# Kernel optimization log

Hardware: AMD Instinct MI355X
Metric: run time of the kernel (lower is better)

Reference implementation:

```python
import jax, jax.numpy as jnp
import numpy as np

N = 100000
IN_C = 256
OUT_C = 256
E = 500000


def gcn_conv(x, W, b, edges):
    """PyG GCNConv: add self-loops, symmetric D^-1/2 (A+I) D^-1/2 normalization,
    then scatter-add of transformed source features into targets, plus bias."""
    n = x.shape[0]
    loop = jnp.arange(n, dtype=edges.dtype)
    row = jnp.concatenate([edges[0], loop])  # source
    col = jnp.concatenate([edges[1], loop])  # target
    deg = jax.ops.segment_sum(jnp.ones_like(col, dtype=x.dtype), col, num_segments=n)
    dis = jax.lax.rsqrt(deg)  # deg >= 1 after self-loops
    norm = dis[row] * dis[col]  # [E+n]
    h = x @ W  # [n, out]
    msg = h[row] * norm[:, None]  # gather + scale
    return jax.ops.segment_sum(msg, col, num_segments=n) + b


def setup_inputs() -> dict:
    key = jax.random.key(0)
    ks = jax.random.split(key, 24)
    x = jax.random.normal(ks[0], (N, IN_C), dtype=jnp.float32)
    edges00 = jax.random.randint(ks[1], (2, E), 0, N, dtype=jnp.int32)
    edges01 = jax.random.randint(ks[2], (2, E), 0, N, dtype=jnp.int32)
    edges10 = jax.random.randint(ks[3], (2, E), 0, N, dtype=jnp.int32)
    edges11 = jax.random.randint(ks[4], (2, E), 0, N, dtype=jnp.int32)
    t0 = (jax.random.uniform(ks[5], (N,)) > 0.5).astype(jnp.float32)
    t1 = 1.0 - t0
    scale = 1.0 / np.sqrt(IN_C)
    W1 = jax.random.normal(ks[6], (IN_C, OUT_C), dtype=jnp.float32) * scale
    W2 = jax.random.normal(ks[7], (IN_C, OUT_C), dtype=jnp.float32) * scale
    W3 = jax.random.normal(ks[8], (IN_C, OUT_C), dtype=jnp.float32) * scale
    W4 = jax.random.normal(ks[9], (IN_C, OUT_C), dtype=jnp.float32) * scale
    b1 = jnp.zeros((OUT_C,), jnp.float32)
    b2 = jnp.zeros((OUT_C,), jnp.float32)
    b3 = jnp.zeros((OUT_C,), jnp.float32)
    b4 = jnp.zeros((OUT_C,), jnp.float32)
    p0 = jax.random.normal(ks[10], (OUT_C,), dtype=jnp.float32)
    p1 = jax.random.normal(ks[11], (OUT_C,), dtype=jnp.float32)
    p2 = jax.random.normal(ks[12], (OUT_C,), dtype=jnp.float32)
    p3 = jax.random.normal(ks[13], (OUT_C,), dtype=jnp.float32)
    p4 = jax.random.normal(ks[14], (OUT_C,), dtype=jnp.float32)
    p5 = jax.random.normal(ks[15], (OUT_C,), dtype=jnp.float32)
    return dict(x=x, edges00=edges00, edges01=edges01, edges10=edges10, edges11=edges11,
                type0_idx=t0, type1_idx=t1,
                W1=W1, b1=b1, W2=W2, b2=b2, W3=W3, b3=b3, W4=W4, b4=b4,
                p0=p0, p1=p1, p2=p2, p3=p3, p4=p4, p5=p5)


def reference(x, edges00, edges01, edges10, edges11, type0_idx, type1_idx,
              W1, b1, W2, b2, W3, b3, W4, b4, p0, p1, p2, p3, p4, p5):
    # x0/x1: first feature column masked by node type, broadcast over out channels
    x0c = type0_idx * x[:, 0]  # [N]
    x1c = type1_idx * x[:, 0]
    x00 = gcn_conv(x, W1, b1, edges00)
    x01 = gcn_conv(x, W2, b2, edges01)
    x10 = gcn_conv(x, W3, b3, edges10)
    x11 = gcn_conv(x, W4, b4, edges11)
    out = (x0c[:, None] * p0 + x1c[:, None] * p1
           + x00 * p2 + x01 * p3 + x10 * p4 + x11 * p5)
    return out
```

## Files before the change

kernel.cpp:

```cpp
#include <hip/hip_runtime.h>


#define PCAP 24

typedef __bf16 v8bf __attribute__((ext_vector_type(8)));
typedef float v4f __attribute__((ext_vector_type(4)));

__device__ __forceinline__ unsigned short f2bf(float f) {
  unsigned u = __float_as_uint(f);
  u += 0x7fffu + ((u >> 16) & 1u);
  return (unsigned short)(u >> 16);
}
__device__ __forceinline__ float bf2f(unsigned short s) {
  return __uint_as_float(((unsigned)s) << 16);
}
__device__ __forceinline__ void async_ld16(const void* g, void* l) {
  __builtin_amdgcn_global_load_lds((__attribute__((address_space(1))) void*)g,
                                   (__attribute__((address_space(3))) void*)l,
                                   16, 0, 0);
}

__global__ void lc_hist(const int* __restrict__ e0, const int* __restrict__ e1,
                        const int* __restrict__ e2, const int* __restrict__ e3,
                        int* __restrict__ deg, int N, int E) {
  int e = blockIdx.x * 256 + threadIdx.x;
  if (e >= E) return;
  int k = blockIdx.y;
  const int* ed = (k == 0) ? e0 : (k == 1) ? e1 : (k == 2) ? e2 : e3;
  int col = ed[E + e];
  atomicAdd(&deg[k * N + col], 1);
}

__global__ void lc_fill(const int* __restrict__ e0, const int* __restrict__ e1,
                        const int* __restrict__ e2, const int* __restrict__ e3,
                        const int* __restrict__ deg, int* __restrict__ cursor,
                        unsigned* __restrict__ payload, int N, int E) {
  int e = blockIdx.x * 256 + threadIdx.x;
  if (e >= E) return;
  int k = blockIdx.y;
  const int* ed = (k == 0) ? e0 : (k == 1) ? e1 : (k == 2) ? e2 : e3;
  int src = ed[e], col = ed[E + e];
  int idx = k * N + col;
  int pos = atomicAdd(&cursor[idx], 1);
  if (pos < PCAP) {
    float ds = rsqrtf((float)(deg[(size_t)k * N + src] + 1));
    unsigned q = (unsigned)(ds * 32767.0f + 0.5f);
    payload[(size_t)idx * PCAP + pos] = (q << 17) | (unsigned)src;
  }
}

__global__ void lc_prep(const float* __restrict__ W1, const float* __restrict__ W2,
                        const float* __restrict__ W3, const float* __restrict__ W4,
                        const float* __restrict__ b1, const float* __restrict__ b2,
                        const float* __restrict__ b3, const float* __restrict__ b4,
                        const float* __restrict__ p2, const float* __restrict__ p3,
                        const float* __restrict__ p4, const float* __restrict__ p5,
                        unsigned short* __restrict__ Wt, float* __restrict__ biasc) {
  __shared__ float tile[256][33];
  int k = blockIdx.y, co0 = blockIdx.x * 32;
  int t = threadIdx.x;
  const float* W = (k == 0) ? W1 : (k == 1) ? W2 : (k == 2) ? W3 : W4;
  const float* p = (k == 0) ? p2 : (k == 1) ? p3 : (k == 2) ? p4 : p5;

  if (blockIdx.x == 0 && k == 0) {
    int c = t;
    biasc[c] = b1[c] * p2[c] + b2[c] * p3[c] + b3[c] * p4[c] + b4[c] * p5[c];
  }

  int coL = t & 31, kkB = t >> 5;
#pragma unroll 4
  for (int pass = 0; pass < 32; ++pass) {
    int kk = pass * 8 + kkB;
    tile[kk][coL] = W[kk * 256 + co0 + coL];
  }
  __syncthreads();

  int co = t >> 3, seg0 = t & 7;
  float pv = p[co0 + co];
#pragma unroll
  for (int i = 0; i < 4; ++i) {
    int s = seg0 + 8 * i;
    ushort4 lo, hi;
    int kk = s * 8;
    lo.x = f2bf(tile[kk + 0][co] * pv); lo.y = f2bf(tile[kk + 1][co] * pv);
    lo.z = f2bf(tile[kk + 2][co] * pv); lo.w = f2bf(tile[kk + 3][co] * pv);
    hi.x = f2bf(tile[kk + 4][co] * pv); hi.y = f2bf(tile[kk + 5][co] * pv);
    hi.z = f2bf(tile[kk + 6][co] * pv); hi.w = f2bf(tile[kk + 7][co] * pv);
    unsigned short* dst = Wt + (size_t)(co0 + co) * 1024 + k * 256 + kk;
    *(ushort4*)dst = lo;
    *(ushort4*)(dst + 4) = hi;
  }
}

__global__ void lc_cvt(const float4* __restrict__ x4, ushort4* __restrict__ xb4,
                       const float* __restrict__ t0, const float* __restrict__ t1,
                       float* __restrict__ m0, float* __restrict__ m1, int n4) {
  int i = blockIdx.x * 256 + threadIdx.x;
  if (i >= n4) return;
  float4 v = x4[i];
  ushort4 r;
  r.x = f2bf(v.x); r.y = f2bf(v.y); r.z = f2bf(v.z); r.w = f2bf(v.w);
  xb4[i] = r;
  if ((i & 63) == 0) {
    int n = i >> 6;
    float xc = v.x;
    m0[n] = t0[n] * xc;
    m1[n] = t1[n] * xc;
  }
}

#define GATP(BASE, POS, LIM, CNT, DNS, A0, A1, A2, A3)                  \
  do {                                                                  \
    int jj = ((POS) < (CNT)) ? (POS) : (LIM);                           \
    unsigned pv = payload[(BASE) + jj];                                 \
    unsigned ss = pv & 0x1FFFFu;                                        \
    ushort4 gg = *(const ushort4*)&xb[(size_t)ss * 256 + c];            \
    float nn = ((POS) < (CNT)) ? (float)(pv >> 17) * (DNS) : 0.f;       \
    A0 += bf2f(gg.x) * nn;                                              \
    A1 += bf2f(gg.y) * nn;                                              \
    A2 += bf2f(gg.z) * nn;                                              \
    A3 += bf2f(gg.w) * nn;                                              \
  } while (0)

__global__ __launch_bounds__(256) void lc_aggx(
    const unsigned short* __restrict__ xb, unsigned short* __restrict__ Agg,
    int aggw, int kcount, int kbase, const int* __restrict__ deg,
    const unsigned* __restrict__ payload, int N) {
  int t = threadIdx.x;
  int w = t >> 6, lane = t & 63;
  int n0, k, koff;
  if (kcount == 4) { n0 = blockIdx.x * 2; k = w; koff = k * 256; }
  else { n0 = blockIdx.x * 8 + w * 2; k = kbase; koff = 0; }
  if (n0 >= N) return;
  int c = lane * 4;
  int n1 = n0 + 1;
  int n1c = (n1 < N) ? n1 : N - 1;
  int idx0 = k * N + n0;
  int idx1 = k * N + n1c;

  int dg0 = deg[idx0], dg1 = deg[idx1];
  float dn0 = rsqrtf((float)(dg0 + 1)), dn1 = rsqrtf((float)(dg1 + 1));
  float dns0 = dn0 * (1.0f / 32767.0f), dns1 = dn1 * (1.0f / 32767.0f);
  float s0 = dn0 * dn0, s1 = dn1 * dn1;
  ushort4 h0 = *(const ushort4*)&xb[(size_t)n0 * 256 + c];
  ushort4 h1 = *(const ushort4*)&xb[(size_t)n1c * 256 + c];
  float a0 = bf2f(h0.x) * s0, a1 = bf2f(h0.y) * s0;
  float a2 = bf2f(h0.z) * s0, a3 = bf2f(h0.w) * s0;
  float u0 = bf2f(h1.x) * s1, u1 = bf2f(h1.y) * s1;
  float u2 = bf2f(h1.z) * s1, u3 = bf2f(h1.w) * s1;

  size_t st0 = (size_t)idx0 * PCAP, st1 = (size_t)idx1 * PCAP;
  int cnt0 = (dg0 > PCAP) ? PCAP : dg0;
  int cnt1 = (dg1 > PCAP) ? PCAP : dg1;
  int lim0 = (cnt0 > 0) ? cnt0 - 1 : 0;
  int lim1 = (cnt1 > 0) ? cnt1 - 1 : 0;
  int cmax = (cnt0 > cnt1) ? cnt0 : cnt1;
  for (int i = 0; i < cmax; i += 4) {
    GATP(st0, i + 0, lim0, cnt0, dns0, a0, a1, a2, a3);
    GATP(st0, i + 1, lim0, cnt0, dns0, a0, a1, a2, a3);
    GATP(st0, i + 2, lim0, cnt0, dns0, a0, a1, a2, a3);
    GATP(st0, i + 3, lim0, cnt0, dns0, a0, a1, a2, a3);
    GATP(st1, i + 0, lim1, cnt1, dns1, u0, u1, u2, u3);
    GATP(st1, i + 1, lim1, cnt1, dns1, u0, u1, u2, u3);
    GATP(st1, i + 2, lim1, cnt1, dns1, u0, u1, u2, u3);
    GATP(st1, i + 3, lim1, cnt1, dns1, u0, u1, u2, u3);
  }

  ushort4 r0, r1;
  r0.x = f2bf(a0); r0.y = f2bf(a1); r0.z = f2bf(a2); r0.w = f2bf(a3);
  r1.x = f2bf(u0); r1.y = f2bf(u1); r1.z = f2bf(u2); r1.w = f2bf(u3);
  *(ushort4*)&Agg[(size_t)n0 * aggw + koff + c] = r0;
  if (n1 < N) *(ushort4*)&Agg[(size_t)n1 * aggw + koff + c] = r1;
}

__global__ __launch_bounds__(512) void lc_gemm(
    const unsigned short* __restrict__ A, int strideA,
    const unsigned short* __restrict__ B, int strideB, int K,
    float* __restrict__ out, int Mrows, int addprev, int doepi,
    const float* __restrict__ m0, const float* __restrict__ m1,
    const float* __restrict__ p0, const float* __restrict__ p1,
    const float* __restrict__ biasc) {
  __shared__ alignas(16) unsigned short As[2][128 * 32];
  __shared__ alignas(16) unsigned short Bs[2][256 * 32];
  int t = threadIdx.x;
  int w = t >> 6, lane = t & 63;
  int wm = w & 1, wn = w >> 1;
  int quad = lane >> 4, l16 = lane & 15;
  int row0 = blockIdx.x * 128;

  v4f acc[4][4];
#pragma unroll
  for (int mt = 0; mt < 4; mt++)
#pragma unroll
    for (int nt = 0; nt < 4; nt++) {
      v4f z = {0.f, 0.f, 0.f, 0.f};
      acc[mt][nt] = z;
    }

  const int ra = t >> 2;
  const int e0 = (t & 3) * 8;
  const int sws = (ra & 3) << 3;
  const unsigned swf = (unsigned)((l16 & 3) << 3);

  int growA = row0 + ra;
  if (growA >= Mrows) growA = Mrows - 1;
  const unsigned short* Ap = A + (size_t)growA * strideA + (e0 ^ sws);
  const unsigned short* Bp0 = B + (size_t)ra * strideB + (e0 ^ sws);
  const unsigned short* Bp1 = B + (size_t)(128 + ra) * strideB + (e0 ^ sws);
  const int lA = ra * 32 + e0;
  const int lB0 = ra * 32 + e0, lB1 = (128 + ra) * 32 + e0;

  async_ld16(Ap, &As[0][lA]);
  async_ld16(Bp0, &Bs[0][lB0]);
  async_ld16(Bp1, &Bs[0][lB1]);
  asm volatile("s_waitcnt vmcnt(0)" ::: "memory");
  __builtin_amdgcn_s_barrier();

  int cur = 0;
  for (int kk = 0; kk < K; kk += 32) {
    if (kk + 32 < K) {
      async_ld16(Ap + kk + 32, &As[cur ^ 1][lA]);
      async_ld16(Bp0 + kk + 32, &Bs[cur ^ 1][lB0]);
      async_ld16(Bp1 + kk + 32, &Bs[cur ^ 1][lB1]);
    }

    v8bf af[4], bfr[4];
    unsigned eq = ((unsigned)(quad * 8)) ^ swf;
#pragma unroll
    for (int mt = 0; mt < 4; mt++) {
      int r = wm * 64 + mt * 16 + l16;
      af[mt] = *(const v8bf*)&As[cur][(unsigned)r * 32 + eq];
    }
#pragma unroll
    for (int nt = 0; nt < 4; nt++) {
      int n = wn * 64 + nt * 16 + l16;
      bfr[nt] = *(const v8bf*)&Bs[cur][(unsigned)n * 32 + eq];
    }
#pragma unroll
    for (int mt = 0; mt < 4; mt++)
#pragma unroll
      for (int nt = 0; nt < 4; nt++)
        acc[mt][nt] =
            __builtin_amdgcn_mfma_f32_16x16x32_bf16(af[mt], bfr[nt], acc[mt][nt], 0, 0, 0);

    asm volatile("s_waitcnt vmcnt(0)" ::: "memory");
    __builtin_amdgcn_s_barrier();
    cur ^= 1;
  }

  float pc0[4], pc1[4], bc[4];
#pragma unroll
  for (int nt = 0; nt < 4; nt++) {
    int gcol = wn * 64 + nt * 16 + l16;
    pc0[nt] = doepi ? p0[gcol] : 0.f;
    pc1[nt] = doepi ? p1[gcol] : 0.f;
    bc[nt] = doepi ? biasc[gcol] : 0.f;
  }
#pragma unroll
  for (int mt = 0; mt < 4; mt++)
#pragma unroll
    for (int r = 0; r < 4; r++) {
      int grow = row0 + wm * 64 + mt * 16 + quad * 4 + r;
      if (grow >= Mrows) continue;
      float m0v = 0.f, m1v = 0.f;
      if (doepi) { m0v = m0[grow]; m1v = m1[grow]; }
#pragma unroll
      for (int nt = 0; nt < 4; nt++) {
        int gcol = wn * 64 + nt * 16 + l16;
        size_t o = (size_t)grow * 256 + gcol;
        float v = acc[mt][nt][r];
        if (addprev) v += out[o];
        if (doepi) v += m0v * pc0[nt] + m1v * pc1[nt] + bc[nt];
        out[o] = v;
      }
    }
}

extern "C" void kernel_launch(void* const* d_in, const int* in_sizes, int n_in,
                              void* d_out, int out_size, void* d_ws, size_t ws_size,
                              hipStream_t stream) {
  const float* x = (const float*)d_in[0];
  const int* e00 = (const int*)d_in[1];
  const int* e01 = (const int*)d_in[2];
  const int* e10 = (const int*)d_in[3];
  const int* e11 = (const int*)d_in[4];
  const float* t0 = (const float*)d_in[5];
  const float* t1 = (const float*)d_in[6];
  const float* W1 = (const float*)d_in[7];
  const float* b1 = (const float*)d_in[8];
  const float* W2 = (const float*)d_in[9];
  const float* b2 = (const float*)d_in[10];
  const float* W3 = (const float*)d_in[11];
  const float* b3 = (const float*)d_in[12];
  const float* W4 = (const float*)d_in[13];
  const float* b4 = (const float*)d_in[14];
  const float* p0 = (const float*)d_in[15];
  const float* p1 = (const float*)d_in[16];
  const float* p2 = (const float*)d_in[17];
  const float* p3 = (const float*)d_in[18];
  const float* p4 = (const float*)d_in[19];
  const float* p5 = (const float*)d_in[20];
  float* out = (float*)d_out;

  int N = in_sizes[0] / 256;
  int E = in_sizes[1] / 2;
  int M4 = 4 * N;

  char* wp = (char*)d_ws;
  auto carve = [&](size_t bytes) {
    void* r = (void*)wp;
    wp += (bytes + 255) & ~(size_t)255;
    return r;
  };
  unsigned short* xb = (unsigned short*)carve((size_t)N * 256 * 2);
  unsigned short* Wt = (unsigned short*)carve((size_t)256 * 1024 * 2);
  int* deg = (int*)carve((size_t)M4 * 4);
  int* cursor = (int*)carve((size_t)M4 * 4);
  float* biasc = (float*)carve(256 * 4);
  float* m0 = (float*)carve((size_t)N * 4);
  float* m1 = (float*)carve((size_t)N * 4);
  unsigned* payload = (unsigned*)carve((size_t)M4 * PCAP * 4);
  size_t used = (size_t)(wp - (char*)d_ws);
  size_t remain = (ws_size > used) ? ws_size - used : 0;
  bool fat = remain >= (size_t)N * 1024 * 2;
  unsigned short* Agg = (unsigned short*)wp;

  int gE = (E + 255) / 256;

  hipMemsetAsync(deg, 0, (size_t)2 * M4 * 4, stream);
  lc_hist<<<dim3(gE, 4), 256, 0, stream>>>(e00, e01, e10, e11, deg, N, E);
  lc_fill<<<dim3(gE, 4), 256, 0, stream>>>(e00, e01, e10, e11, deg, cursor,
                                           payload, N, E);
  lc_prep<<<dim3(8, 4), 256, 0, stream>>>(W1, W2, W3, W4, b1, b2, b3, b4,
                                          p2, p3, p4, p5, Wt, biasc);
  lc_cvt<<<(N * 64 + 255) / 256, 256, 0, stream>>>((const float4*)x, (ushort4*)xb,
                                                   t0, t1, m0, m1, N * 64);

  int gemm_mb = (N + 127) / 128;
  if (fat) {
    lc_aggx<<<(N + 1) / 2, 256, 0, stream>>>(xb, Agg, 1024, 4, 0, deg, payload, N);
    lc_gemm<<<gemm_mb, 512, 0, stream>>>(Agg, 1024, Wt, 1024, 1024, out, N,
                                         0, 1, m0, m1, p0, p1, biasc);
  } else {
    for (int k = 0; k < 4; k++) {
      lc_aggx<<<(N + 7) / 8, 256, 0, stream>>>(xb, Agg, 256, 1, k, deg, payload, N);
      lc_gemm<<<gemm_mb, 512, 0, stream>>>(Agg, 256, Wt + k * 256, 1024, 256,
                                           out, N, (k > 0) ? 1 : 0,
                                           (k == 3) ? 1 : 0, m0, m1, p0, p1,
                                           biasc);
    }
  }
}
```

Measured before the change: 690.6 us.

## Merge preprocessing kernels into one launch and triple-buffer GEMM loads

The histogram, bf16 conversion and weight-prep kernels are folded into a single launch that dispatches work by block index, removing two kernel launches. The weight transpose now uses one block per output column with strided, uncoalesced reads instead of an LDS tile. The GEMM moves from a double-buffered to a triple-buffered LDS pipeline with partial vmcnt waits, so loads run two tiles ahead. This uses more shared memory per block, which may reduce occupancy.

```diff
diff --git a/kernel.cpp b/kernel.cpp
--- a/kernel.cpp
+++ b/kernel.cpp
@@ -20,15 +20,57 @@
                                    16, 0, 0);
 }
 
-__global__ void lc_hist(const int* __restrict__ e0, const int* __restrict__ e1,
-                        const int* __restrict__ e2, const int* __restrict__ e3,
-                        int* __restrict__ deg, int N, int E) {
-  int e = blockIdx.x * 256 + threadIdx.x;
-  if (e >= E) return;
-  int k = blockIdx.y;
-  const int* ed = (k == 0) ? e0 : (k == 1) ? e1 : (k == 2) ? e2 : e3;
-  int col = ed[E + e];
-  atomicAdd(&deg[k * N + col], 1);
+__global__ void lc_pre(const int* __restrict__ e0, const int* __restrict__ e1,
+                       const int* __restrict__ e2, const int* __restrict__ e3,
+                       int* __restrict__ deg, int N, int E, int gE,
+                       const float4* __restrict__ x4, ushort4* __restrict__ xb4,
+                       const float* __restrict__ t0, const float* __restrict__ t1,
+                       float* __restrict__ m0, float* __restrict__ m1,
+                       const float* __restrict__ W1, const float* __restrict__ W2,
+                       const float* __restrict__ W3, const float* __restrict__ W4,
+                       const float* __restrict__ b1, const float* __restrict__ b2,
+                       const float* __restrict__ b3, const float* __restrict__ b4,
+                       const float* __restrict__ p2, const float* __restrict__ p3,
+                       const float* __restrict__ p4, const float* __restrict__ p5,
+                       unsigned short* __restrict__ Wt, float* __restrict__ biasc) {
+  int b = blockIdx.x;
+  int tid = threadIdx.x;
+  int HB = 4 * gE;
+  int CB = (N * 64 + 255) / 256;
+
+  if (b < HB) {
+    int k = b / gE;
+    int e = (b - k * gE) * 256 + tid;
+    if (e >= E) return;
+    const int* ed = (k == 0) ? e0 : (k == 1) ? e1 : (k == 2) ? e2 : e3;
+    atomicAdd(&deg[k * N + ed[E + e]], 1);
+    return;
+  }
+  b -= HB;
+  if (b < CB) {
+    int i = b * 256 + tid;
+    if (i >= N * 64) return;
+    float4 v = x4[i];
+    ushort4 r;
+    r.x = f2bf(v.x); r.y = f2bf(v.y); r.z = f2bf(v.z); r.w = f2bf(v.w);
+    xb4[i] = r;
+    if ((i & 63) == 0) {
+      int n = i >> 6;
+      float xc = v.x;
+      m0[n] = t0[n] * xc;
+      m1[n] = t1[n] * xc;
+    }
+    return;
+  }
+  b -= CB;
+  int k = b >> 8, co = b & 255;
+  const float* W = (k == 0) ? W1 : (k == 1) ? W2 : (k == 2) ? W3 : W4;
+  const float* p = (k == 0) ? p2 : (k == 1) ? p3 : (k == 2) ? p4 : p5;
+  Wt[(size_t)co * 1024 + k * 256 + tid] = f2bf(W[tid * 256 + co] * p[co]);
+  if (b == 0) {
+    int c = tid;
+    biasc[c] = b1[c] * p2[c] + b2[c] * p3[c] + b3[c] * p4[c] + b4[c] * p5[c];
+  }
 }
 
 __global__ void lc_fill(const int* __restrict__ e0, const int* __restrict__ e1,
@@ -49,66 +91,6 @@
   }
 }
 
-__global__ void lc_prep(const float* __restrict__ W1, const float* __restrict__ W2,
-                        const float* __restrict__ W3, const float* __restrict__ W4,
-                        const float* __restrict__ b1, const float* __restrict__ b2,
-                        const float* __restrict__ b3, const float* __restrict__ b4,
-                        const float* __restrict__ p2, const float* __restrict__ p3,
-                        const float* __restrict__ p4, const float* __restrict__ p5,
-                        unsigned short* __restrict__ Wt, float* __restrict__ biasc) {
-  __shared__ float tile[256][33];
-  int k = blockIdx.y, co0 = blockIdx.x * 32;
-  int t = threadIdx.x;
-  const float* W = (k == 0) ? W1 : (k == 1) ? W2 : (k == 2) ? W3 : W4;
-  const float* p = (k == 0) ? p2 : (k == 1) ? p3 : (k == 2) ? p4 : p5;
-
-  if (blockIdx.x == 0 && k == 0) {
-    int c = t;
-    biasc[c] = b1[c] * p2[c] + b2[c] * p3[c] + b3[c] * p4[c] + b4[c] * p5[c];
-  }
-
-  int coL = t & 31, kkB = t >> 5;
-#pragma unroll 4
-  for (int pass = 0; pass < 32; ++pass) {
-    int kk = pass * 8 + kkB;
-    tile[kk][coL] = W[kk * 256 + co0 + coL];
-  }
-  __syncthreads();
-
-  int co = t >> 3, seg0 = t & 7;
-  float pv = p[co0 + co];
-#pragma unroll
-  for (int i = 0; i < 4; ++i) {
-    int s = seg0 + 8 * i;
-    ushort4 lo, hi;
-    int kk = s * 8;
-    lo.x = f2bf(tile[kk + 0][co] * pv); lo.y = f2bf(tile[kk + 1][co] * pv);
-    lo.z = f2bf(tile[kk + 2][co] * pv); lo.w = f2bf(tile[kk + 3][co] * pv);
-    hi.x = f2bf(tile[kk + 4][co] * pv); hi.y = f2bf(tile[kk + 5][co] * pv);
-    hi.z = f2bf(tile[kk + 6][co] * pv); hi.w = f2bf(tile[kk + 7][co] * pv);
-    unsigned short* dst = Wt + (size_t)(co0 + co) * 1024 + k * 256 + kk;
-    *(ushort4*)dst = lo;
-    *(ushort4*)(dst + 4) = hi;
-  }
-}
-
-__global__ void lc_cvt(const float4* __restrict__ x4, ushort4* __restrict__ xb4,
-                       const float* __restrict__ t0, const float* __restrict__ t1,
-                       float* __restrict__ m0, float* __restrict__ m1, int n4) {
-  int i = blockIdx.x * 256 + threadIdx.x;
-  if (i >= n4) return;
-  float4 v = x4[i];
-  ushort4 r;
-  r.x = f2bf(v.x); r.y = f2bf(v.y); r.z = f2bf(v.z); r.w = f2bf(v.w);
-  xb4[i] = r;
-  if ((i & 63) == 0) {
-    int n = i >> 6;
-    float xc = v.x;
-    m0[n] = t0[n] * xc;
-    m1[n] = t1[n] * xc;
-  }
-}
-
 #define GATP(BASE, POS, LIM, CNT, DNS, A0, A1, A2, A3)                  \
   do {                                                                  \
     int jj = ((POS) < (CNT)) ? (POS) : (LIM);                           \
@@ -180,8 +162,8 @@
     const float* __restrict__ m0, const float* __restrict__ m1,
     const float* __restrict__ p0, const float* __restrict__ p1,
     const float* __restrict__ biasc) {
-  __shared__ alignas(16) unsigned short As[2][128 * 32];
-  __shared__ alignas(16) unsigned short Bs[2][256 * 32];
+  __shared__ alignas(16) unsigned short As[3][128 * 32];
+  __shared__ alignas(16) unsigned short Bs[3][256 * 32];
   int t = threadIdx.x;
   int w = t >> 6, lane = t & 63;
   int wm = w & 1, wn = w >> 1;
@@ -210,31 +192,39 @@
   const int lA = ra * 32 + e0;
   const int lB0 = ra * 32 + e0, lB1 = (128 + ra) * 32 + e0;
 
-  async_ld16(Ap, &As[0][lA]);
-  async_ld16(Bp0, &Bs[0][lB0]);
-  async_ld16(Bp1, &Bs[0][lB1]);
-  asm volatile("s_waitcnt vmcnt(0)" ::: "memory");
-  __builtin_amdgcn_s_barrier();
-
-  int cur = 0;
-  for (int kk = 0; kk < K; kk += 32) {
-    if (kk + 32 < K) {
-      async_ld16(Ap + kk + 32, &As[cur ^ 1][lA]);
-      async_ld16(Bp0 + kk + 32, &Bs[cur ^ 1][lB0]);
-      async_ld16(Bp1 + kk + 32, &Bs[cur ^ 1][lB1]);
-    }
+  const int T = K >> 5;
+  auto STAGE = [&](int tt, int bi) {
+    async_ld16(Ap + tt * 32, &As[bi][lA]);
+    async_ld16(Bp0 + tt * 32, &Bs[bi][lB0]);
+    async_ld16(Bp1 + tt * 32, &Bs[bi][lB1]);
+  };
+
+  STAGE(0, 0);
+  if (T > 1) STAGE(1, 1);
+
+  int bt = 0;
+  for (int tix = 0; tix < T; ++tix) {
+    if (tix + 2 < T) {
+      int bn = bt + 2; if (bn >= 3) bn -= 3;
+      STAGE(tix + 2, bn);
+    }
+    int ahead = ((tix + 2 < T) ? 2 : (tix + 1 < T) ? 1 : 0);
+    if (ahead == 2) asm volatile("s_waitcnt vmcnt(6)" ::: "memory");
+    else if (ahead == 1) asm volatile("s_waitcnt vmcnt(3)" ::: "memory");
+    else asm volatile("s_waitcnt vmcnt(0)" ::: "memory");
+    __builtin_amdgcn_s_barrier();
 
     v8bf af[4], bfr[4];
     unsigned eq = ((unsigned)(quad * 8)) ^ swf;
 #pragma unroll
     for (int mt = 0; mt < 4; mt++) {
       int r = wm * 64 + mt * 16 + l16;
-      af[mt] = *(const v8bf*)&As[cur][(unsigned)r * 32 + eq];
+      af[mt] = *(const v8bf*)&As[bt][(unsigned)r * 32 + eq];
     }
 #pragma unroll
     for (int nt = 0; nt < 4; nt++) {
       int n = wn * 64 + nt * 16 + l16;
-      bfr[nt] = *(const v8bf*)&Bs[cur][(unsigned)n * 32 + eq];
+      bfr[nt] = *(const v8bf*)&Bs[bt][(unsigned)n * 32 + eq];
     }
 #pragma unroll
     for (int mt = 0; mt < 4; mt++)
@@ -243,9 +233,8 @@
         acc[mt][nt] =
             __builtin_amdgcn_mfma_f32_16x16x32_bf16(af[mt], bfr[nt], acc[mt][nt], 0, 0, 0);
 
-    asm volatile("s_waitcnt vmcnt(0)" ::: "memory");
     __builtin_amdgcn_s_barrier();
-    cur ^= 1;
+    ++bt; if (bt == 3) bt = 0;
   }
 
   float pc0[4], pc1[4], bc[4];
@@ -326,15 +315,17 @@
   unsigned short* Agg = (unsigned short*)wp;
 
   int gE = (E + 255) / 256;
+  int HB = 4 * gE;
+  int CB = (N * 64 + 255) / 256;
+  int preblocks = HB + CB + 1024;
 
   hipMemsetAsync(deg, 0, (size_t)2 * M4 * 4, stream);
-  lc_hist<<<dim3(gE, 4), 256, 0, stream>>>(e00, e01, e10, e11, deg, N, E);
+  lc_pre<<<preblocks, 256, 0, stream>>>(e00, e01, e10, e11, deg, N, E, gE,
+                                        (const float4*)x, (ushort4*)xb, t0, t1,
+                                        m0, m1, W1, W2, W3, W4, b1, b2, b3, b4,
+                                        p2, p3, p4, p5, Wt, biasc);
   lc_fill<<<dim3(gE, 4), 256, 0, stream>>>(e00, e01, e10, e11, deg, cursor,
                                            payload, N, E);
-  lc_prep<<<dim3(8, 4), 256, 0, stream>>>(W1, W2, W3, W4, b1, b2, b3, b4,
-                                          p2, p3, p4, p5, Wt, biasc);
-  lc_cvt<<<(N * 64 + 255) / 256, 256, 0, stream>>>((const float4*)x, (ushort4*)xb,
-                                                   t0, t1, m0, m1, N * 64);
 
   int gemm_mb = (N + 127) / 128;
   if (fat) {
```

Result: no change. 696.0 us (+0.8%).
